# Optimization experiments

Measured on AMD Instinct MI355X. Metric: run time of the kernel, lower is better.

## Reference

```python
import jax, jax.numpy as jnp
import numpy as np

D_MODEL = 1024
N_HEADS = 16
HEAD_DIM = D_MODEL // N_HEADS


def setup_inputs() -> dict:
    key = jax.random.key(0)
    ks = jax.random.split(key, 11)
    B, S = 4, 2048
    scale = 1.0 / np.sqrt(D_MODEL)
    inp = {
        "query": jax.random.normal(ks[0], (B, S, D_MODEL), jnp.float32),
        "key": jax.random.normal(ks[1], (B, S, D_MODEL), jnp.float32),
        "value": jax.random.normal(ks[2], (B, S, D_MODEL), jnp.float32),
        "Wq": jax.random.normal(ks[3], (D_MODEL, D_MODEL), jnp.float32) * scale,
        "bq": jnp.zeros((D_MODEL,), jnp.float32),
        "Wk": jax.random.normal(ks[4], (D_MODEL, D_MODEL), jnp.float32) * scale,
        "bk": jnp.zeros((D_MODEL,), jnp.float32),
        "Wv": jax.random.normal(ks[5], (D_MODEL, D_MODEL), jnp.float32) * scale,
        "bv": jnp.zeros((D_MODEL,), jnp.float32),
        "Wo": jax.random.normal(ks[6], (D_MODEL, D_MODEL), jnp.float32) * scale,
        "bo": jnp.zeros((D_MODEL,), jnp.float32),
    }
    return inp


def reference(query, key, value, Wq, bq, Wk, bk, Wv, bv, Wo, bo):
    B, S, _ = query.shape
    # QKV projections (nn.Linear: x @ W.T + b; weights here stored as [out,in])
    q = query @ Wq.T + bq
    k = key @ Wk.T + bk
    v = value @ Wv.T + bv
    # [B, S, H, Dh] -> [B, H, S, Dh]
    q = q.reshape(B, S, N_HEADS, HEAD_DIM).transpose(0, 2, 1, 3)
    k = k.reshape(B, S, N_HEADS, HEAD_DIM).transpose(0, 2, 1, 3)
    v = v.reshape(B, S, N_HEADS, HEAD_DIM).transpose(0, 2, 1, 3)
    # full score matrix [B, H, S, S]
    scores = jnp.einsum("bhqd,bhkd->bhqk", q, k) / jnp.sqrt(
        jnp.asarray(HEAD_DIM, q.dtype)
    )
    attn = jax.nn.softmax(scores, axis=-1)
    out = jnp.einsum("bhqk,bhkd->bhqd", attn, v)  # [B, H, S, Dh]
    out = out.transpose(0, 2, 1, 3).reshape(B, S, D_MODEL)
    return out @ Wo.T + bo
```

## Files before the change

### kernel.cpp

```cpp
#include <hip/hip_runtime.h>
#include <cstdint>
#include <cstddef>


typedef _Float16 h16;
typedef _Float16 h16x4 __attribute__((ext_vector_type(4)));
typedef _Float16 h16x8 __attribute__((ext_vector_type(8)));
typedef float f32x4 __attribute__((ext_vector_type(4)));
typedef float f32x16 __attribute__((ext_vector_type(16)));

#define SEQ 2048
#define HDIM 64

__device__ __forceinline__ void gld16(const void* g, void* l) {
  __builtin_amdgcn_global_load_lds((__attribute__((address_space(1))) void*)g,
                                   (__attribute__((address_space(3))) void*)l,
                                   16, 0, 0);
}

#define VMCNT_(n) asm volatile("s_waitcnt vmcnt(" #n ")" ::: "memory")
#define VMCNT(n) VMCNT_(n)

struct CvtArgs {
  const float* src[7];
  h16* dst[7];
  int n4[7];
};

__global__ __launch_bounds__(256) void cvt_kernel(CvtArgs a) {
  const int tk = blockIdx.y;
  const int n4 = a.n4[tk];
  const float4* s = (const float4*)a.src[tk];
  h16x4* d = (h16x4*)a.dst[tk];
  const int stride = gridDim.x * blockDim.x;
  for (int i = blockIdx.x * blockDim.x + threadIdx.x; i < n4; i += stride) {
    float4 v = s[i];
    h16x4 o = {(h16)v.x, (h16)v.y, (h16)v.z, (h16)v.w};
    d[i] = o;
  }
}

enum { EPI_QK = 0, EPI_V = 1, EPI_OUT = 2 };

struct GemmArgs {
  const h16* A[3];
  const h16* W[3];
  const float* bias[3];
  void* dst[3];
  float scale[3];
  int epi[3];
};

__global__ __launch_bounds__(512, 2) void gemm256(GemmArgs g) {
  extern __shared__ __align__(16) h16 lds[];

  const int z = blockIdx.z;
  const h16* __restrict__ A = g.A[z];
  const h16* __restrict__ W = g.W[z];
  const float* __restrict__ bias = g.bias[z];
  void* dst = g.dst[z];
  const float scale = g.scale[z];
  const int epi = g.epi[z];

  int bid = blockIdx.y * 4 + blockIdx.x;
  bid = (bid & 7) * 16 + (bid >> 3);
  const int m0 = (bid >> 2) * 256;
  const int n0 = (bid & 3) * 256;

  const int t = threadIdx.x;
  const int lane = t & 63, wave = t >> 6;
  const int lq = lane & 15, quad = lane >> 4;
  const int wm = wave >> 2, wn = wave & 3;

  const int l2 = lane >> 2;
  const int qsw = (lane & 3) ^ ((lane >> 3) & 3);
  const h16* gA0 = A + (size_t)(m0 + (wave * 2 + 0) * 16 + l2) * 1024 + qsw * 8;
  const h16* gA1 = A + (size_t)(m0 + (wave * 2 + 1) * 16 + l2) * 1024 + qsw * 8;
  const h16* gB0 = W + (size_t)(n0 + (wave * 2 + 0) * 16 + l2) * 1024 + qsw * 8;
  const h16* gB1 = W + (size_t)(n0 + (wave * 2 + 1) * 16 + l2) * 1024 + qsw * 8;
  h16* ldsA0 = &lds[(wave * 2 + 0) * 512];
  h16* ldsA1 = &lds[(wave * 2 + 1) * 512];
  h16* ldsB0 = &lds[8192 + (wave * 2 + 0) * 512];
  h16* ldsB1 = &lds[8192 + (wave * 2 + 1) * 512];

  const int swr = quad ^ ((lq >> 1) & 3);
  const int aRd = (wm * 128 + lq) * 32 + swr * 8;
  const int bRd = 8192 + (wn * 64 + lq) * 32 + swr * 8;

  f32x4 acc[8][4];
  f32x4 zero4 = {0.f, 0.f, 0.f, 0.f};
#pragma unroll
  for (int i = 0; i < 8; ++i)
#pragma unroll
    for (int j = 0; j < 4; ++j) acc[i][j] = zero4;

#pragma unroll
  for (int s = 0; s < 3; ++s) {
    gld16(gA0 + s * 32, ldsA0 + s * 16384);
    gld16(gB0 + s * 32, ldsB0 + s * 16384);
    gld16(gA1 + s * 32, ldsA1 + s * 16384);
    gld16(gB1 + s * 32, ldsB1 + s * 16384);
  }

#define SUBTILE(SLOT, STK, DO_STAGE, VM)                                      \
  {                                                                           \
    VMCNT(VM);                                                                \
    __builtin_amdgcn_s_barrier();                                             \
    __builtin_amdgcn_sched_barrier(0);                                        \
    const h16* aS = &lds[(SLOT) * 16384 + aRd];                               \
    const h16* bS = &lds[(SLOT) * 16384 + bRd];                               \
    h16x8 af0[4], bf[4], af1[4];                                              \
    _Pragma("unroll") for (int i = 0; i < 4; ++i) {                           \
      af0[i] = *(const h16x8*)(aS + i * 512);                                 \
    }                                                                         \
    _Pragma("unroll") for (int i = 0; i < 4; ++i) {                           \
      bf[i] = *(const h16x8*)(bS + i * 512);                                  \
    }                                                                         \
    if (DO_STAGE) {                                                           \
      gld16(gA0 + (STK), ldsA0 + ((SLOT + 3) & 3) * 16384);                   \
      gld16(gB0 + (STK), ldsB0 + ((SLOT + 3) & 3) * 16384);                   \
    }                                                                         \
    __builtin_amdgcn_s_setprio(1);                                            \
    _Pragma("unroll") for (int i = 0; i < 4; ++i) {                           \
      _Pragma("unroll") for (int j = 0; j < 4; ++j) {                         \
        acc[i][j] = __builtin_amdgcn_mfma_f32_16x16x32_f16(af0[i], bf[j],     \
                                                           acc[i][j], 0, 0, 0);\
      }                                                                       \
    }                                                                         \
    __builtin_amdgcn_s_setprio(0);                                            \
    _Pragma("unroll") for (int i = 0; i < 4; ++i) {                           \
      af1[i] = *(const h16x8*)(aS + (4 + i) * 512);                           \
    }                                                                         \
    if (DO_STAGE) {                                                           \
      gld16(gA1 + (STK), ldsA1 + ((SLOT + 3) & 3) * 16384);                   \
      gld16(gB1 + (STK), ldsB1 + ((SLOT + 3) & 3) * 16384);                   \
    }                                                                         \
    __builtin_amdgcn_s_setprio(1);                                            \
    _Pragma("unroll") for (int i = 0; i < 4; ++i) {                           \
      _Pragma("unroll") for (int j = 0; j < 4; ++j) {                         \
        acc[4 + i][j] = __builtin_amdgcn_mfma_f32_16x16x32_f16(               \
            af1[i], bf[j], acc[4 + i][j], 0, 0, 0);                           \
      }                                                                       \
    }                                                                         \
    __builtin_amdgcn_s_setprio(0);                                            \
  }

  int kb = 0;
#pragma unroll 1
  for (int s4 = 0; s4 < 7; ++s4, kb += 128) {
    SUBTILE(0, kb + 96, true, 8);
    SUBTILE(1, kb + 128, true, 8);
    SUBTILE(2, kb + 160, true, 8);
    SUBTILE(3, kb + 192, true, 8);
  }
  SUBTILE(0, 992, true, 8);
  SUBTILE(1, 0, false, 8);
  SUBTILE(2, 0, false, 4);
  SUBTILE(3, 0, false, 0);
#undef SUBTILE

  const int gmb = m0 + wm * 128;
  const int gnb = n0 + wn * 64;
#pragma unroll
  for (int mf = 0; mf < 8; ++mf) {
#pragma unroll
    for (int nf = 0; nf < 4; ++nf) {
      const int gn = gnb + nf * 16 + lq;
      const float bv = bias[gn];
#pragma unroll
      for (int r = 0; r < 4; ++r) {
        const int gm = gmb + mf * 16 + quad * 4 + r;
        const float v = (acc[mf][nf][r] + bv) * scale;
        if (epi == EPI_OUT) {
          ((float*)dst)[(size_t)gm * 1024 + gn] = v;
        } else if (epi == EPI_QK) {
          const int b = gm >> 11, s = gm & 2047, h = gn >> 6, d = gn & 63;
          ((h16*)dst)[((size_t)(b * 16 + h) * 2048 + s) * 64 + d] = (h16)v;
        } else {
          const int b = gm >> 11, s = gm & 2047, h = gn >> 6, d = gn & 63;
          ((h16*)dst)[((size_t)(b * 16 + h) * 64 + d) * 2048 + s] = (h16)v;
        }
      }
    }
  }
}

__global__ __launch_bounds__(256, 4) void flash_fwd(
    const h16* __restrict__ Qp, const h16* __restrict__ Kp,
    const h16* __restrict__ Vtp, h16* __restrict__ attn) {
  __shared__ __align__(16) h16 sK[128 * 72];
  __shared__ __align__(16) h16 sVt[64 * 136];

  const int t = threadIdx.x, lane = t & 63, wave = t >> 6;
  const int l31 = lane & 31;
  const int h = lane >> 5;
  const int bh = blockIdx.y, q0 = blockIdx.x * 128;

  const h16* Qh = Qp + (size_t)bh * SEQ * HDIM;
  const h16* Kh = Kp + (size_t)bh * SEQ * HDIM;
  const h16* Vh = Vtp + (size_t)bh * HDIM * SEQ;

  const int qrow = q0 + wave * 32 + l31;
  h16x8 bq[4];
#pragma unroll
  for (int ks = 0; ks < 4; ++ks)
    bq[ks] = *(const h16x8*)(Qh + (size_t)qrow * 64 + ks * 16 + h * 8);

  f32x16 zero16 = {};
  f32x16 oT[2];
  oT[0] = zero16;
  oT[1] = zero16;
  float lsum = 0.f;

  for (int kt = 0; kt < SEQ; kt += 128) {
    __syncthreads();
#pragma unroll
    for (int p = 0; p < 4; ++p) {
      const int c = t + p * 256;
      const int rowK = c >> 3, colK = (c & 7) * 8;
      *(h16x8*)&sK[rowK * 72 + colK] =
          *(const h16x8*)(Kh + (size_t)(kt + rowK) * 64 + colK);
      const int rowV = c >> 4, colV = (c & 15) * 8;
      *(h16x8*)&sVt[rowV * 136 + colV] =
          *(const h16x8*)(Vh + (size_t)rowV * SEQ + kt + colV);
    }
    __syncthreads();

    uint2 pk[16];
#pragma unroll
    for (int mt = 0; mt < 4; ++mt) {
      f32x16 s = zero16;
#pragma unroll
      for (int ks = 0; ks < 4; ++ks) {
        h16x8 ak = *(const h16x8*)&sK[(mt * 32 + l31) * 72 + ks * 16 + h * 8];
        s = __builtin_amdgcn_mfma_f32_32x32x16_f16(ak, bq[ks], s, 0, 0, 0);
      }
#pragma unroll
      for (int g = 0; g < 4; ++g) {
        const float p0 = __expf(s[g * 4 + 0]);
        const float p1 = __expf(s[g * 4 + 1]);
        const float p2 = __expf(s[g * 4 + 2]);
        const float p3 = __expf(s[g * 4 + 3]);
        lsum += (p0 + p1) + (p2 + p3);
        h16x4 q4 = {(h16)p0, (h16)p1, (h16)p2, (h16)p3};
        pk[mt * 4 + g] = __builtin_bit_cast(uint2, q4);
      }
    }

#pragma unroll
    for (int ks = 0; ks < 8; ++ks) {
      const uint2 a = pk[2 * ks];
      const uint2 b = pk[2 * ks + 1];
      uint2 send;
      send.x = h ? a.x : b.x;
      send.y = h ? a.y : b.y;
      uint2 recv;
      recv.x = (unsigned)__shfl_xor((int)send.x, 32);
      recv.y = (unsigned)__shfl_xor((int)send.y, 32);
      uint2 lo, hi;
      lo.x = h ? recv.x : a.x;
      lo.y = h ? recv.y : a.y;
      hi.x = h ? b.x : recv.x;
      hi.y = h ? b.y : recv.y;
      uint4 bp32 = {lo.x, lo.y, hi.x, hi.y};
      h16x8 bp = __builtin_bit_cast(h16x8, bp32);
#pragma unroll
      for (int dt = 0; dt < 2; ++dt) {
        h16x8 av =
            *(const h16x8*)&sVt[(dt * 32 + l31) * 136 + ks * 16 + h * 8];
        oT[dt] = __builtin_amdgcn_mfma_f32_32x32x16_f16(av, bp, oT[dt], 0, 0, 0);
      }
    }
  }

  lsum += __shfl_xor(lsum, 32);
  const float inv = 1.f / lsum;

  const int b = bh >> 4, head = bh & 15;
  h16* orow = attn + ((size_t)(b * SEQ + qrow)) * 1024 + head * 64;
#pragma unroll
  for (int dt = 0; dt < 2; ++dt) {
#pragma unroll
    for (int g = 0; g < 4; ++g) {
      h16x4 ov = {(h16)(oT[dt][g * 4 + 0] * inv), (h16)(oT[dt][g * 4 + 1] * inv),
                  (h16)(oT[dt][g * 4 + 2] * inv), (h16)(oT[dt][g * 4 + 3] * inv)};
      *(h16x4*)&orow[dt * 32 + g * 8 + h * 4] = ov;
    }
  }
}

extern "C" void kernel_launch(void* const* d_in, const int* in_sizes, int n_in,
                              void* d_out, int out_size, void* d_ws,
                              size_t ws_size, hipStream_t stream) {
  (void)in_sizes; (void)n_in; (void)out_size;

  const float* query = (const float*)d_in[0];
  const float* key   = (const float*)d_in[1];
  const float* value = (const float*)d_in[2];
  const float* Wq = (const float*)d_in[3];
  const float* bq = (const float*)d_in[4];
  const float* Wk = (const float*)d_in[5];
  const float* bk = (const float*)d_in[6];
  const float* Wv = (const float*)d_in[7];
  const float* bv = (const float*)d_in[8];
  const float* Wo = (const float*)d_in[9];
  const float* bo = (const float*)d_in[10];

  char* ws = (char*)d_ws;
  const size_t MB = 1024 * 1024;
  h16* xq = (h16*)(ws);
  h16* xk = (h16*)(ws + 16 * MB);
  h16* xv = (h16*)(ws + 32 * MB);
  h16* qperm = (h16*)(ws + 48 * MB);
  h16 *kperm, *vperm, *attn, *w16;
  const bool fused = ws_size >= 104 * MB;
  if (fused) {
    kperm = (h16*)(ws + 64 * MB);
    vperm = (h16*)(ws + 80 * MB);
    w16   = (h16*)(ws + 96 * MB);
    attn  = (h16*)(ws);
  } else {
    kperm = (h16*)(ws);
    vperm = (h16*)(ws + 16 * MB);
    attn  = (h16*)(ws + 32 * MB);
    w16   = (h16*)(ws + 64 * MB);
  }
  h16* wq16 = w16;
  h16* wk16 = w16 + 1048576;
  h16* wv16 = w16 + 2 * 1048576;
  h16* wo16 = w16 + 3 * 1048576;

  static bool attr_set = false;
  if (!attr_set) {
    (void)hipFuncSetAttribute((const void*)gemm256,
                              hipFuncAttributeMaxDynamicSharedMemorySize,
                              131072);
    attr_set = true;
  }

  CvtArgs ca;
  const float* csrc[7] = {query, key, value, Wq, Wk, Wv, Wo};
  h16* cdst[7] = {xq, xk, xv, wq16, wk16, wv16, wo16};
  const int cn4[7] = {2097152, 2097152, 2097152, 262144, 262144, 262144, 262144};
  for (int i = 0; i < 7; ++i) { ca.src[i] = csrc[i]; ca.dst[i] = cdst[i]; ca.n4[i] = cn4[i]; }
  cvt_kernel<<<dim3(512, 7), 256, 0, stream>>>(ca);

  if (fused) {
    GemmArgs ga;
    ga.A[0] = xq; ga.A[1] = xk; ga.A[2] = xv;
    ga.W[0] = wq16; ga.W[1] = wk16; ga.W[2] = wv16;
    ga.bias[0] = bq; ga.bias[1] = bk; ga.bias[2] = bv;
    ga.dst[0] = qperm; ga.dst[1] = kperm; ga.dst[2] = vperm;
    ga.scale[0] = 0.125f; ga.scale[1] = 1.f; ga.scale[2] = 1.f;
    ga.epi[0] = EPI_QK; ga.epi[1] = EPI_QK; ga.epi[2] = EPI_V;
    gemm256<<<dim3(4, 32, 3), 512, 131072, stream>>>(ga);
  } else {
    const h16* As[3] = {xq, xk, xv};
    const h16* Ws[3] = {wq16, wk16, wv16};
    const float* bs[3] = {bq, bk, bv};
    h16* ds[3] = {qperm, kperm, vperm};
    const float scl[3] = {0.125f, 1.f, 1.f};
    const int ep[3] = {EPI_QK, EPI_QK, EPI_V};
    for (int i = 0; i < 3; ++i) {
      GemmArgs ga;
      for (int j = 0; j < 3; ++j) {
        ga.A[j] = As[i]; ga.W[j] = Ws[i]; ga.bias[j] = bs[i];
        ga.dst[j] = ds[i]; ga.scale[j] = scl[i]; ga.epi[j] = ep[i];
      }
      gemm256<<<dim3(4, 32, 1), 512, 131072, stream>>>(ga);
    }
  }

  flash_fwd<<<dim3(16, 64), 256, 0, stream>>>(qperm, kperm, vperm, attn);

  GemmArgs go;
  for (int j = 0; j < 3; ++j) {
    go.A[j] = attn; go.W[j] = wo16; go.bias[j] = bo;
    go.dst[j] = d_out; go.scale[j] = 1.f; go.epi[j] = EPI_OUT;
  }
  gemm256<<<dim3(4, 32, 1), 512, 131072, stream>>>(go);
}
```

Baseline: 408.8 us.

## Template GEMM tile width, prefetch K/V in flash kernel, fold log2e into Q scale

The GEMM becomes a template over the N tile width. The output projection uses a 128-wide tile with 256 blocks instead of 128, to fill more CUs, and block ids are remapped across the whole grid. The flash attention kernel now register-prefetches the next K/V tile while computing on the current one, raises wave priority around the MFMA blocks, and swizzles its block order. It also replaces __expf with exp2f by folding log2(e) into the Q projection scale. These changes target poor occupancy in the out-projection GEMM and exposed global-load latency in attention, at the cost of more registers in the flash kernel.

After: 474.3 us. 16.0% more time.

```diff
diff --git a/kernel.cpp b/kernel.cpp
--- a/kernel.cpp
+++ b/kernel.cpp
@@ -51,10 +51,25 @@
   int epi[3];
 };
 
-__global__ __launch_bounds__(512, 2) void gemm256(GemmArgs g) {
+template <int BN>
+__global__ __launch_bounds__(512, 2) void gemm_t(GemmArgs g) {
+  constexpr int NT = 1024 / BN;
+  constexpr int NF = BN / 64;
+  constexpr int ASZ = 8192;
+  constexpr int SLOTH = ASZ + BN * 32;
+  constexpr int PT = 32 * NT;
+
   extern __shared__ __align__(16) h16 lds[];
 
-  const int z = blockIdx.z;
+  const int lin =
+      blockIdx.x + gridDim.x * (blockIdx.y + gridDim.y * blockIdx.z);
+  const int total = gridDim.x * gridDim.y * gridDim.z;
+  const int nid = (lin & 7) * (total >> 3) + (lin >> 3);
+  const int z = nid / PT;
+  const int r = nid % PT;
+  const int m0 = (r / NT) * 256;
+  const int n0 = (r % NT) * BN;
+
   const h16* __restrict__ A = g.A[z];
   const h16* __restrict__ W = g.W[z];
   const float* __restrict__ bias = g.bias[z];
@@ -62,11 +77,6 @@
   const float scale = g.scale[z];
   const int epi = g.epi[z];
 
-  int bid = blockIdx.y * 4 + blockIdx.x;
-  bid = (bid & 7) * 16 + (bid >> 3);
-  const int m0 = (bid >> 2) * 256;
-  const int n0 = (bid & 3) * 256;
-
   const int t = threadIdx.x;
   const int lane = t & 63, wave = t >> 6;
   const int lq = lane & 15, quad = lane >> 4;
@@ -74,32 +84,33 @@
 
   const int l2 = lane >> 2;
   const int qsw = (lane & 3) ^ ((lane >> 3) & 3);
-  const h16* gA0 = A + (size_t)(m0 + (wave * 2 + 0) * 16 + l2) * 1024 + qsw * 8;
-  const h16* gA1 = A + (size_t)(m0 + (wave * 2 + 1) * 16 + l2) * 1024 + qsw * 8;
-  const h16* gB0 = W + (size_t)(n0 + (wave * 2 + 0) * 16 + l2) * 1024 + qsw * 8;
-  const h16* gB1 = W + (size_t)(n0 + (wave * 2 + 1) * 16 + l2) * 1024 + qsw * 8;
-  h16* ldsA0 = &lds[(wave * 2 + 0) * 512];
-  h16* ldsA1 = &lds[(wave * 2 + 1) * 512];
-  h16* ldsB0 = &lds[8192 + (wave * 2 + 0) * 512];
-  h16* ldsB1 = &lds[8192 + (wave * 2 + 1) * 512];
+  const h16* gA0 = A + (size_t)(m0 + wave * 32 + l2) * 1024 + qsw * 8;
+  const h16* gA1 = gA0 + 16 * 1024;
+  const h16* gB0 =
+      W + (size_t)(n0 + wave * (BN == 256 ? 32 : 16) + l2) * 1024 + qsw * 8;
+  const h16* gB1 = gB0 + 16 * 1024;
+  h16* ldsA0 = &lds[wave * 2 * 512];
+  h16* ldsA1 = ldsA0 + 512;
+  h16* ldsB0 = &lds[ASZ + wave * (BN == 256 ? 2 : 1) * 512];
+  h16* ldsB1 = ldsB0 + 512;
 
   const int swr = quad ^ ((lq >> 1) & 3);
   const int aRd = (wm * 128 + lq) * 32 + swr * 8;
-  const int bRd = 8192 + (wn * 64 + lq) * 32 + swr * 8;
-
-  f32x4 acc[8][4];
+  const int bRd = ASZ + (wn * (NF * 16) + lq) * 32 + swr * 8;
+
+  f32x4 acc[8][NF];
   f32x4 zero4 = {0.f, 0.f, 0.f, 0.f};
 #pragma unroll
   for (int i = 0; i < 8; ++i)
 #pragma unroll
-    for (int j = 0; j < 4; ++j) acc[i][j] = zero4;
+    for (int j = 0; j < NF; ++j) acc[i][j] = zero4;
 
 #pragma unroll
   for (int s = 0; s < 3; ++s) {
-    gld16(gA0 + s * 32, ldsA0 + s * 16384);
-    gld16(gB0 + s * 32, ldsB0 + s * 16384);
-    gld16(gA1 + s * 32, ldsA1 + s * 16384);
-    gld16(gB1 + s * 32, ldsB1 + s * 16384);
+    gld16(gA0 + s * 32, ldsA0 + s * SLOTH);
+    gld16(gB0 + s * 32, ldsB0 + s * SLOTH);
+    gld16(gA1 + s * 32, ldsA1 + s * SLOTH);
+    if constexpr (BN == 256) gld16(gB1 + s * 32, ldsB1 + s * SLOTH);
   }
 
 #define SUBTILE(SLOT, STK, DO_STAGE, VM)                                      \
@@ -107,22 +118,22 @@
     VMCNT(VM);                                                                \
     __builtin_amdgcn_s_barrier();                                             \
     __builtin_amdgcn_sched_barrier(0);                                        \
-    const h16* aS = &lds[(SLOT) * 16384 + aRd];                               \
-    const h16* bS = &lds[(SLOT) * 16384 + bRd];                               \
-    h16x8 af0[4], bf[4], af1[4];                                              \
+    const h16* aS = &lds[(SLOT) * SLOTH + aRd];                               \
+    const h16* bS = &lds[(SLOT) * SLOTH + bRd];                               \
+    h16x8 af0[4], bf[NF], af1[4];                                             \
     _Pragma("unroll") for (int i = 0; i < 4; ++i) {                           \
       af0[i] = *(const h16x8*)(aS + i * 512);                                 \
     }                                                                         \
-    _Pragma("unroll") for (int i = 0; i < 4; ++i) {                           \
-      bf[i] = *(const h16x8*)(bS + i * 512);                                  \
+    _Pragma("unroll") for (int j = 0; j < NF; ++j) {                          \
+      bf[j] = *(const h16x8*)(bS + j * 512);                                  \
     }                                                                         \
     if (DO_STAGE) {                                                           \
-      gld16(gA0 + (STK), ldsA0 + ((SLOT + 3) & 3) * 16384);                   \
-      gld16(gB0 + (STK), ldsB0 + ((SLOT + 3) & 3) * 16384);                   \
+      gld16(gA0 + (STK), ldsA0 + ((SLOT + 3) & 3) * SLOTH);                   \
+      gld16(gB0 + (STK), ldsB0 + ((SLOT + 3) & 3) * SLOTH);                   \
     }                                                                         \
     __builtin_amdgcn_s_setprio(1);                                            \
     _Pragma("unroll") for (int i = 0; i < 4; ++i) {                           \
-      _Pragma("unroll") for (int j = 0; j < 4; ++j) {                         \
+      _Pragma("unroll") for (int j = 0; j < NF; ++j) {                        \
         acc[i][j] = __builtin_amdgcn_mfma_f32_16x16x32_f16(af0[i], bf[j],     \
                                                            acc[i][j], 0, 0, 0);\
       }                                                                       \
@@ -132,12 +143,13 @@
       af1[i] = *(const h16x8*)(aS + (4 + i) * 512);                           \
     }                                                                         \
     if (DO_STAGE) {                                                           \
-      gld16(gA1 + (STK), ldsA1 + ((SLOT + 3) & 3) * 16384);                   \
-      gld16(gB1 + (STK), ldsB1 + ((SLOT + 3) & 3) * 16384);                   \
+      gld16(gA1 + (STK), ldsA1 + ((SLOT + 3) & 3) * SLOTH);                   \
+      if constexpr (BN == 256)                                                \
+        gld16(gB1 + (STK), ldsB1 + ((SLOT + 3) & 3) * SLOTH);                 \
     }                                                                         \
     __builtin_amdgcn_s_setprio(1);                                            \
     _Pragma("unroll") for (int i = 0; i < 4; ++i) {                           \
-      _Pragma("unroll") for (int j = 0; j < 4; ++j) {                         \
+      _Pragma("unroll") for (int j = 0; j < NF; ++j) {                        \
         acc[4 + i][j] = __builtin_amdgcn_mfma_f32_16x16x32_f16(               \
             af1[i], bf[j], acc[4 + i][j], 0, 0, 0);                           \
       }                                                                       \
@@ -146,31 +158,45 @@
   }
 
   int kb = 0;
+  if constexpr (BN == 256) {
 #pragma unroll 1
-  for (int s4 = 0; s4 < 7; ++s4, kb += 128) {
-    SUBTILE(0, kb + 96, true, 8);
-    SUBTILE(1, kb + 128, true, 8);
-    SUBTILE(2, kb + 160, true, 8);
-    SUBTILE(3, kb + 192, true, 8);
-  }
-  SUBTILE(0, 992, true, 8);
-  SUBTILE(1, 0, false, 8);
-  SUBTILE(2, 0, false, 4);
-  SUBTILE(3, 0, false, 0);
+    for (int s4 = 0; s4 < 7; ++s4, kb += 128) {
+      SUBTILE(0, kb + 96, true, 8);
+      SUBTILE(1, kb + 128, true, 8);
+      SUBTILE(2, kb + 160, true, 8);
+      SUBTILE(3, kb + 192, true, 8);
+    }
+    SUBTILE(0, 992, true, 8);
+    SUBTILE(1, 0, false, 8);
+    SUBTILE(2, 0, false, 4);
+    SUBTILE(3, 0, false, 0);
+  } else {
+#pragma unroll 1
+    for (int s4 = 0; s4 < 7; ++s4, kb += 128) {
+      SUBTILE(0, kb + 96, true, 6);
+      SUBTILE(1, kb + 128, true, 6);
+      SUBTILE(2, kb + 160, true, 6);
+      SUBTILE(3, kb + 192, true, 6);
+    }
+    SUBTILE(0, 992, true, 6);
+    SUBTILE(1, 0, false, 6);
+    SUBTILE(2, 0, false, 3);
+    SUBTILE(3, 0, false, 0);
+  }
 #undef SUBTILE
 
   const int gmb = m0 + wm * 128;
-  const int gnb = n0 + wn * 64;
+  const int gnb = n0 + wn * (NF * 16);
 #pragma unroll
   for (int mf = 0; mf < 8; ++mf) {
 #pragma unroll
-    for (int nf = 0; nf < 4; ++nf) {
+    for (int nf = 0; nf < NF; ++nf) {
       const int gn = gnb + nf * 16 + lq;
       const float bv = bias[gn];
 #pragma unroll
-      for (int r = 0; r < 4; ++r) {
-        const int gm = gmb + mf * 16 + quad * 4 + r;
-        const float v = (acc[mf][nf][r] + bv) * scale;
+      for (int rr = 0; rr < 4; ++rr) {
+        const int gm = gmb + mf * 16 + quad * 4 + rr;
+        const float v = (acc[mf][nf][rr] + bv) * scale;
         if (epi == EPI_OUT) {
           ((float*)dst)[(size_t)gm * 1024 + gn] = v;
         } else if (epi == EPI_QK) {
@@ -194,7 +220,10 @@
   const int t = threadIdx.x, lane = t & 63, wave = t >> 6;
   const int l31 = lane & 31;
   const int h = lane >> 5;
-  const int bh = blockIdx.y, q0 = blockIdx.x * 128;
+
+  const int lin = blockIdx.x + (blockIdx.y << 4);
+  const int nid = (lin & 7) * 128 + (lin >> 3);
+  const int bh = nid >> 4, q0 = (nid & 15) * 128;
 
   const h16* Qh = Qp + (size_t)bh * SEQ * HDIM;
   const h16* Kh = Kp + (size_t)bh * SEQ * HDIM;
@@ -205,6 +234,14 @@
 #pragma unroll
   for (int ks = 0; ks < 4; ++ks)
     bq[ks] = *(const h16x8*)(Qh + (size_t)qrow * 64 + ks * 16 + h * 8);
+
+  h16x8 kreg[4], vreg[4];
+#pragma unroll
+  for (int p = 0; p < 4; ++p) {
+    const int c = t + p * 256;
+    kreg[p] = *(const h16x8*)(Kh + (size_t)(c >> 3) * 64 + (c & 7) * 8);
+    vreg[p] = *(const h16x8*)(Vh + (size_t)(c >> 4) * SEQ + (c & 15) * 8);
+  }
 
   f32x16 zero16 = {};
   f32x16 oT[2];
@@ -217,30 +254,41 @@
 #pragma unroll
     for (int p = 0; p < 4; ++p) {
       const int c = t + p * 256;
-      const int rowK = c >> 3, colK = (c & 7) * 8;
-      *(h16x8*)&sK[rowK * 72 + colK] =
-          *(const h16x8*)(Kh + (size_t)(kt + rowK) * 64 + colK);
-      const int rowV = c >> 4, colV = (c & 15) * 8;
-      *(h16x8*)&sVt[rowV * 136 + colV] =
-          *(const h16x8*)(Vh + (size_t)rowV * SEQ + kt + colV);
+      *(h16x8*)&sK[(c >> 3) * 72 + (c & 7) * 8] = kreg[p];
+      *(h16x8*)&sVt[(c >> 4) * 136 + (c & 15) * 8] = vreg[p];
     }
     __syncthreads();
+
+    if (kt + 128 < SEQ) {
+#pragma unroll
+      for (int p = 0; p < 4; ++p) {
+        const int c = t + p * 256;
+        kreg[p] = *(const h16x8*)(Kh +
+                                  (size_t)(kt + 128 + (c >> 3)) * 64 +
+                                  (c & 7) * 8);
+        vreg[p] = *(const h16x8*)(Vh + (size_t)(c >> 4) * SEQ + kt + 128 +
+                                  (c & 15) * 8);
+      }
+    }
+    __builtin_amdgcn_sched_barrier(0);
 
     uint2 pk[16];
 #pragma unroll
     for (int mt = 0; mt < 4; ++mt) {
       f32x16 s = zero16;
+      __builtin_amdgcn_s_setprio(1);
 #pragma unroll
       for (int ks = 0; ks < 4; ++ks) {
         h16x8 ak = *(const h16x8*)&sK[(mt * 32 + l31) * 72 + ks * 16 + h * 8];
         s = __builtin_amdgcn_mfma_f32_32x32x16_f16(ak, bq[ks], s, 0, 0, 0);
       }
+      __builtin_amdgcn_s_setprio(0);
 #pragma unroll
       for (int g = 0; g < 4; ++g) {
-        const float p0 = __expf(s[g * 4 + 0]);
-        const float p1 = __expf(s[g * 4 + 1]);
-        const float p2 = __expf(s[g * 4 + 2]);
-        const float p3 = __expf(s[g * 4 + 3]);
+        const float p0 = exp2f(s[g * 4 + 0]);
+        const float p1 = exp2f(s[g * 4 + 1]);
+        const float p2 = exp2f(s[g * 4 + 2]);
+        const float p3 = exp2f(s[g * 4 + 3]);
         lsum += (p0 + p1) + (p2 + p3);
         h16x4 q4 = {(h16)p0, (h16)p1, (h16)p2, (h16)p3};
         pk[mt * 4 + g] = __builtin_bit_cast(uint2, q4);
@@ -264,12 +312,14 @@
       hi.y = h ? b.y : recv.y;
       uint4 bp32 = {lo.x, lo.y, hi.x, hi.y};
       h16x8 bp = __builtin_bit_cast(h16x8, bp32);
+      __builtin_amdgcn_s_setprio(1);
 #pragma unroll
       for (int dt = 0; dt < 2; ++dt) {
         h16x8 av =
             *(const h16x8*)&sVt[(dt * 32 + l31) * 136 + ks * 16 + h * 8];
         oT[dt] = __builtin_amdgcn_mfma_f32_32x32x16_f16(av, bp, oT[dt], 0, 0, 0);
       }
+      __builtin_amdgcn_s_setprio(0);
     }
   }
 
@@ -332,9 +382,12 @@
 
   static bool attr_set = false;
   if (!attr_set) {
-    (void)hipFuncSetAttribute((const void*)gemm256,
+    (void)hipFuncSetAttribute((const void*)gemm_t<256>,
                               hipFuncAttributeMaxDynamicSharedMemorySize,
                               131072);
+    (void)hipFuncSetAttribute((const void*)gemm_t<128>,
+                              hipFuncAttributeMaxDynamicSharedMemorySize,
+                              98304);
     attr_set = true;
   }
 
@@ -345,21 +398,22 @@
   for (int i = 0; i < 7; ++i) { ca.src[i] = csrc[i]; ca.dst[i] = cdst[i]; ca.n4[i] = cn4[i]; }
   cvt_kernel<<<dim3(512, 7), 256, 0, stream>>>(ca);
 
+  const float qscale = 0.125f * 1.4426950408889634f;
   if (fused) {
     GemmArgs ga;
     ga.A[0] = xq; ga.A[1] = xk; ga.A[2] = xv;
     ga.W[0] = wq16; ga.W[1] = wk16; ga.W[2] = wv16;
     ga.bias[0] = bq; ga.bias[1] = bk; ga.bias[2] = bv;
     ga.dst[0] = qperm; ga.dst[1] = kperm; ga.dst[2] = vperm;
-    ga.scale[0] = 0.125f; ga.scale[1] = 1.f; ga.scale[2] = 1.f;
+    ga.scale[0] = qscale; ga.scale[1] = 1.f; ga.scale[2] = 1.f;
     ga.epi[0] = EPI_QK; ga.epi[1] = EPI_QK; ga.epi[2] = EPI_V;
-    gemm256<<<dim3(4, 32, 3), 512, 131072, stream>>>(ga);
+    gemm_t<256><<<dim3(4, 32, 3), 512, 131072, stream>>>(ga);
   } else {
     const h16* As[3] = {xq, xk, xv};
     const h16* Ws[3] = {wq16, wk16, wv16};
     const float* bs[3] = {bq, bk, bv};
     h16* ds[3] = {qperm, kperm, vperm};
-    const float scl[3] = {0.125f, 1.f, 1.f};
+    const float scl[3] = {qscale, 1.f, 1.f};
     const int ep[3] = {EPI_QK, EPI_QK, EPI_V};
     for (int i = 0; i < 3; ++i) {
       GemmArgs ga;
@@ -367,7 +421,7 @@
         ga.A[j] = As[i]; ga.W[j] = Ws[i]; ga.bias[j] = bs[i];
         ga.dst[j] = ds[i]; ga.scale[j] = scl[i]; ga.epi[j] = ep[i];
       }
-      gemm256<<<dim3(4, 32, 1), 512, 131072, stream>>>(ga);
+      gemm_t<256><<<dim3(4, 32, 1), 512, 131072, stream>>>(ga);
     }
   }
 
@@ -378,5 +432,5 @@
     go.A[j] = attn; go.W[j] = wo16; go.bias[j] = bo;
     go.dst[j] = d_out; go.scale[j] = 1.f; go.epi[j] = EPI_OUT;
   }
-  gemm256<<<dim3(4, 32, 1), 512, 131072, stream>>>(go);
+  gemm_t<128><<<dim3(8, 32, 1), 512, 98304, stream>>>(go);
 }
```
